# Kernel tuning notes

Measured on AMD Instinct MI355X. Metric: run time of the kernel, lower is better.

## Reference

```python
import jax, jax.numpy as jnp
import numpy as np

G_CRYSTALS = 64   # number of crystals in the batch
N_ATOMS = 64      # atoms per crystal (dense n^2 edge block per crystal)
N_HEADS = 8
HEAD_DIM = 64


def _make_edges(g, n):
    # dense all-pairs (i, j) within each crystal; atoms of crystal c occupy [c*n, (c+1)*n)
    base = np.arange(g, dtype=np.int32)[:, None, None] * n   # (G,1,1)
    idx = np.arange(n, dtype=np.int32)
    e0 = np.broadcast_to(base + idx[None, :, None], (g, n, n)).reshape(-1)  # query index
    e1 = np.broadcast_to(base + idx[None, None, :], (g, n, n)).reshape(-1)  # key index
    return jnp.asarray(np.stack([e0, e1], axis=0))  # (2, M)


def setup_inputs() -> dict:
    key = jax.random.key(0)
    k0, k1, k2, k3, k4 = jax.random.split(key, 5)
    N = G_CRYSTALS * N_ATOMS                 # 4096 atoms total
    M = G_CRYSTALS * N_ATOMS * N_ATOMS       # 262144 edges
    q = jax.random.normal(k0, (N, N_HEADS, HEAD_DIM), jnp.float32)
    k = jax.random.normal(k1, (N, N_HEADS, HEAD_DIM), jnp.float32)
    v = jax.random.normal(k2, (N, N_HEADS, HEAD_DIM), jnp.float32)
    attn_weights = jax.random.normal(k3, (M, N_HEADS), jnp.float32)          # per-edge additive bias
    values = jax.random.normal(k4, (M, N_HEADS, HEAD_DIM), jnp.float32) * 0.1  # per-edge fused value term
    edges = _make_edges(G_CRYSTALS, N_ATOMS)
    return {"q": q, "k": k, "v": v, "attn_weights": attn_weights,
            "values": values, "edges": edges}


def reference(q, k, v, attn_weights, values, edges):
    # Faithful to the norm_func_mode==0 ('default') fallback path of
    # _scaled_dot_product_attention: per-edge logits, softmax over keys per
    # query (within each crystal's dense block), fused value term.
    N, H, Dh = q.shape
    e0, e1 = edges[0], edges[1]
    scale = 1.0 / jnp.sqrt(jnp.asarray(Dh, q.dtype))
    # per-edge attention logits: (M, H)
    a = jnp.einsum('mhd,mhd->mh', q[e0] * scale, k[e1]) + attn_weights
    # stable softmax over edges sharing the same query index e0
    m = jax.ops.segment_max(a, e0, num_segments=N)      # (N, H)
    p = jnp.exp(a - m[e0])                              # (M, H)
    denom = jax.ops.segment_sum(p, e0, num_segments=N)  # (N, H)
    w = p / denom[e0]                                   # (M, H)
    # output[i] = sum_j w[ij] * (v[j] + values[ij])
    out = jax.ops.segment_sum(w[:, :, None] * (v[e1] + values), e0, num_segments=N)
    return out  # (N, H, Dh)
```

## Files before the change

### kernel.cpp

```cpp
#include <hip/hip_runtime.h>


#define NH 8
#define HD 64
#define ROWSTRIDE 68

__global__ __launch_bounds__(256, 2)
void crystal_attn_kernel(const float* __restrict__ q,
                         const float* __restrict__ k,
                         const float* __restrict__ v,
                         const float* __restrict__ aw,
                         const float* __restrict__ values,
                         float* __restrict__ out) {
    const int c = blockIdx.x & 63;
    const int h = blockIdx.x >> 6;
    const int t = threadIdx.x;

    __shared__ __align__(16) float sq[64][ROWSTRIDE];
    __shared__ __align__(16) float sk[64][ROWSTRIDE];
    __shared__ __align__(16) float sv[64][ROWSTRIDE];
    __shared__ __align__(16) float sa[64][ROWSTRIDE];
    __shared__ float sden[64];

    {
        const size_t rowbase = ((size_t)c * 64) * (NH * HD) + (size_t)h * HD;
        const float* qg = q + rowbase;
        const float* kg = k + rowbase;
        const float* vg = v + rowbase;
        #pragma unroll
        for (int s = 0; s < 4; ++s) {
            int u   = t + 256 * s;
            int row = u >> 4;
            int col = (u & 15) * 4;
            size_t goff = (size_t)row * (NH * HD) + col;
            *(float4*)&sq[row][col] = *(const float4*)(qg + goff);
            *(float4*)&sk[row][col] = *(const float4*)(kg + goff);
            *(float4*)&sv[row][col] = *(const float4*)(vg + goff);
        }
        const float* ag = aw + ((size_t)c * 4096) * NH + h;
        #pragma unroll
        for (int s = 0; s < 16; ++s) {
            int idx = t + 256 * s;
            sa[idx >> 6][idx & 63] = ag[(size_t)idx * NH];
        }
    }
    __syncthreads();

    {
        const int w = t >> 6;
        const int i = t & 63;
        const int jbase = w * 16;
        float acc[16];
        #pragma unroll
        for (int jj = 0; jj < 16; ++jj) acc[jj] = 0.f;
        #pragma unroll 4
        for (int d4 = 0; d4 < 16; ++d4) {
            float4 qv = *(const float4*)&sq[i][d4 * 4];
            #pragma unroll
            for (int jj = 0; jj < 16; ++jj) {
                float4 kv = *(const float4*)&sk[jbase + jj][d4 * 4];
                acc[jj] += qv.x * kv.x + qv.y * kv.y + qv.z * kv.z + qv.w * kv.w;
            }
        }
        #pragma unroll
        for (int jj = 0; jj < 16; ++jj)
            sa[i][jbase + jj] = acc[jj] * 0.125f + sa[i][jbase + jj];
    }
    __syncthreads();

    {
        const int r  = t >> 2;
        const int jb = (t & 3) * 16;
        float mx = -1e30f;
        #pragma unroll
        for (int jj = 0; jj < 16; ++jj) mx = fmaxf(mx, sa[r][jb + jj]);
        mx = fmaxf(mx, __shfl_xor(mx, 1));
        mx = fmaxf(mx, __shfl_xor(mx, 2));
        float sum = 0.f;
        #pragma unroll
        for (int jj = 0; jj < 16; ++jj) {
            float p = __expf(sa[r][jb + jj] - mx);
            sa[r][jb + jj] = p;
            sum += p;
        }
        sum += __shfl_xor(sum, 1);
        sum += __shfl_xor(sum, 2);
        if ((t & 3) == 0) sden[r] = sum;
    }
    __syncthreads();

    {
        const int w    = t >> 6;
        const int lane = t & 63;
        const int e    = lane >> 4;
        const int dq   = lane & 15;
        const float* vb = values + ((size_t)c * 4096) * (NH * HD) + (size_t)h * HD + dq * 4;
        float* ob = out + ((size_t)c * 64) * (NH * HD) + (size_t)h * HD + dq * 4;
        #pragma unroll
        for (int r = 0; r < 4; ++r) {
            const int i = 16 * w + 4 * r + e;
            const float* vrow = vb + (size_t)i * 64 * (NH * HD);
            float4 acc = make_float4(0.f, 0.f, 0.f, 0.f);
            #pragma unroll 8
            for (int j = 0; j < 64; ++j) {
                float4 val = *(const float4*)(vrow + (size_t)j * (NH * HD));
                float  p   = sa[i][j];
                float4 sj  = *(const float4*)&sv[j][dq * 4];
                acc.x += p * (sj.x + val.x);
                acc.y += p * (sj.y + val.y);
                acc.z += p * (sj.z + val.z);
                acc.w += p * (sj.w + val.w);
            }
            const float inv = 1.0f / sden[i];
            float4 o = make_float4(acc.x * inv, acc.y * inv, acc.z * inv, acc.w * inv);
            *(float4*)(ob + (size_t)i * (NH * HD)) = o;
        }
    }
}

extern "C" void kernel_launch(void* const* d_in, const int* in_sizes, int n_in,
                              void* d_out, int out_size, void* d_ws, size_t ws_size,
                              hipStream_t stream) {
    const float* q      = (const float*)d_in[0];
    const float* k      = (const float*)d_in[1];
    const float* v      = (const float*)d_in[2];
    const float* aw     = (const float*)d_in[3];
    const float* values = (const float*)d_in[4];
    float* out = (float*)d_out;

    dim3 grid(512);
    dim3 block(256);
    hipLaunchKernelGGL(crystal_attn_kernel, grid, block, 0, stream,
                       q, k, v, aw, values, out);
}
```

Measured before the change: 704.0 us.

## Widen blocks to 1024 threads and stream per-edge values with nontemporal loads

Each block now runs 1024 threads instead of 256, so every thread loads one tile element, computes 4 logits instead of 16, and produces one output row segment instead of four. This gives more waves per block to hide latency on the memory-bound 512 MB per-edge values stream. Those values are now read with nontemporal loads to avoid polluting the cache. The risk is that 1024-thread blocks with about 70 KB of LDS each limit how many blocks fit per CU, and the launch bound of 8 may force register spilling.

Result: faster. 688.9 us (-2.1%).

```diff
diff --git a/kernel.cpp b/kernel.cpp
--- a/kernel.cpp
+++ b/kernel.cpp
@@ -5,7 +5,9 @@
 #define HD 64
 #define ROWSTRIDE 68
 
-__global__ __launch_bounds__(256, 2)
+typedef float f4 __attribute__((ext_vector_type(4)));
+
+__global__ __launch_bounds__(1024, 8)
 void crystal_attn_kernel(const float* __restrict__ q,
                          const float* __restrict__ k,
                          const float* __restrict__ v,
@@ -27,20 +29,17 @@
         const float* qg = q + rowbase;
         const float* kg = k + rowbase;
         const float* vg = v + rowbase;
+        const int row = t >> 4;
+        const int col = (t & 15) * 4;
+        const size_t goff = (size_t)row * (NH * HD) + col;
+        *(float4*)&sq[row][col] = *(const float4*)(qg + goff);
+        *(float4*)&sk[row][col] = *(const float4*)(kg + goff);
+        *(float4*)&sv[row][col] = *(const float4*)(vg + goff);
+
+        const float* ag = aw + ((size_t)c * 4096) * NH + h;
         #pragma unroll
         for (int s = 0; s < 4; ++s) {
-            int u   = t + 256 * s;
-            int row = u >> 4;
-            int col = (u & 15) * 4;
-            size_t goff = (size_t)row * (NH * HD) + col;
-            *(float4*)&sq[row][col] = *(const float4*)(qg + goff);
-            *(float4*)&sk[row][col] = *(const float4*)(kg + goff);
-            *(float4*)&sv[row][col] = *(const float4*)(vg + goff);
-        }
-        const float* ag = aw + ((size_t)c * 4096) * NH + h;
-        #pragma unroll
-        for (int s = 0; s < 16; ++s) {
-            int idx = t + 256 * s;
+            int idx = t + 1024 * s;
             sa[idx >> 6][idx & 63] = ag[(size_t)idx * NH];
         }
     }
@@ -49,43 +48,47 @@
     {
         const int w = t >> 6;
         const int i = t & 63;
-        const int jbase = w * 16;
-        float acc[16];
+        const int jbase = w * 4;
+        float acc[4];
         #pragma unroll
-        for (int jj = 0; jj < 16; ++jj) acc[jj] = 0.f;
+        for (int jj = 0; jj < 4; ++jj) acc[jj] = 0.f;
         #pragma unroll 4
         for (int d4 = 0; d4 < 16; ++d4) {
             float4 qv = *(const float4*)&sq[i][d4 * 4];
             #pragma unroll
-            for (int jj = 0; jj < 16; ++jj) {
+            for (int jj = 0; jj < 4; ++jj) {
                 float4 kv = *(const float4*)&sk[jbase + jj][d4 * 4];
                 acc[jj] += qv.x * kv.x + qv.y * kv.y + qv.z * kv.z + qv.w * kv.w;
             }
         }
         #pragma unroll
-        for (int jj = 0; jj < 16; ++jj)
+        for (int jj = 0; jj < 4; ++jj)
             sa[i][jbase + jj] = acc[jj] * 0.125f + sa[i][jbase + jj];
     }
     __syncthreads();
 
     {
-        const int r  = t >> 2;
-        const int jb = (t & 3) * 16;
+        const int r  = t >> 4;
+        const int jb = (t & 15) * 4;
         float mx = -1e30f;
         #pragma unroll
-        for (int jj = 0; jj < 16; ++jj) mx = fmaxf(mx, sa[r][jb + jj]);
+        for (int jj = 0; jj < 4; ++jj) mx = fmaxf(mx, sa[r][jb + jj]);
         mx = fmaxf(mx, __shfl_xor(mx, 1));
         mx = fmaxf(mx, __shfl_xor(mx, 2));
+        mx = fmaxf(mx, __shfl_xor(mx, 4));
+        mx = fmaxf(mx, __shfl_xor(mx, 8));
         float sum = 0.f;
         #pragma unroll
-        for (int jj = 0; jj < 16; ++jj) {
+        for (int jj = 0; jj < 4; ++jj) {
             float p = __expf(sa[r][jb + jj] - mx);
             sa[r][jb + jj] = p;
             sum += p;
         }
         sum += __shfl_xor(sum, 1);
         sum += __shfl_xor(sum, 2);
-        if ((t & 3) == 0) sden[r] = sum;
+        sum += __shfl_xor(sum, 4);
+        sum += __shfl_xor(sum, 8);
+        if ((t & 15) == 0) sden[r] = sum;
     }
     __syncthreads();
 
@@ -94,27 +97,26 @@
         const int lane = t & 63;
         const int e    = lane >> 4;
         const int dq   = lane & 15;
-        const float* vb = values + ((size_t)c * 4096) * (NH * HD) + (size_t)h * HD + dq * 4;
-        float* ob = out + ((size_t)c * 64) * (NH * HD) + (size_t)h * HD + dq * 4;
-        #pragma unroll
-        for (int r = 0; r < 4; ++r) {
-            const int i = 16 * w + 4 * r + e;
-            const float* vrow = vb + (size_t)i * 64 * (NH * HD);
-            float4 acc = make_float4(0.f, 0.f, 0.f, 0.f);
-            #pragma unroll 8
-            for (int j = 0; j < 64; ++j) {
-                float4 val = *(const float4*)(vrow + (size_t)j * (NH * HD));
-                float  p   = sa[i][j];
-                float4 sj  = *(const float4*)&sv[j][dq * 4];
-                acc.x += p * (sj.x + val.x);
-                acc.y += p * (sj.y + val.y);
-                acc.z += p * (sj.z + val.z);
-                acc.w += p * (sj.w + val.w);
-            }
-            const float inv = 1.0f / sden[i];
-            float4 o = make_float4(acc.x * inv, acc.y * inv, acc.z * inv, acc.w * inv);
-            *(float4*)(ob + (size_t)i * (NH * HD)) = o;
+        const int i    = 4 * w + e;
+
+        const float* vrow = values
+            + ((size_t)(c * 4096 + i * 64)) * (NH * HD)
+            + (size_t)h * HD + dq * 4;
+        float4 acc = make_float4(0.f, 0.f, 0.f, 0.f);
+        #pragma unroll 4
+        for (int j = 0; j < 64; ++j) {
+            f4 val = __builtin_nontemporal_load(
+                         (const f4*)(vrow + (size_t)j * (NH * HD)));
+            float  p  = sa[i][j];
+            float4 sj = *(const float4*)&sv[j][dq * 4];
+            acc.x += p * (sj.x + val.x);
+            acc.y += p * (sj.y + val.y);
+            acc.z += p * (sj.z + val.z);
+            acc.w += p * (sj.w + val.w);
         }
+        const float inv = 1.0f / sden[i];
+        float* ob = out + ((size_t)(c * 64 + i)) * (NH * HD) + (size_t)h * HD + dq * 4;
+        *(float4*)ob = make_float4(acc.x * inv, acc.y * inv, acc.z * inv, acc.w * inv);
     }
 }
 
@@ -129,7 +131,7 @@
     float* out = (float*)d_out;
 
     dim3 grid(512);
-    dim3 block(256);
+    dim3 block(1024);
     hipLaunchKernelGGL(crystal_attn_kernel, grid, block, 0, stream,
                        q, k, v, aw, values, out);
 }
```
